# Performance work log

Hardware: AMD Instinct MI355X
Metric: run time of the kernel (lower is better)

Reference implementation:

```python
import jax, jax.numpy as jnp
import numpy as np

N_NODES = 50000
N_EDGES = 800000
IN_CH = 128
OUT_CH = 32
HID = 2 * OUT_CH  # 64


def gcn_layer(x, W, b, src, dst, n):
    """PyG GCNConv: x' = D^-1/2 (A + I) D^-1/2 (x W) + b, flow source->target."""
    h = x @ W  # [n, out]
    # degree on target nodes, +1 for self loop
    deg = jax.ops.segment_sum(jnp.ones(dst.shape[0], h.dtype), dst, num_segments=n) + 1.0
    dis = jax.lax.rsqrt(deg)  # deg^-1/2
    norm = dis[src] * dis[dst]  # [E]
    msg = h[src] * norm[:, None]  # gather + scale, [E, out]
    agg = jax.ops.segment_sum(msg, dst, num_segments=n)  # scatter-add
    # self-loop contribution has norm dis[i]*dis[i] = 1/deg[i]
    return agg + h * (dis * dis)[:, None] + b


def setup_inputs() -> dict:
    key = jax.random.key(0)
    k1, k2, k3, k4, k5, k6 = jax.random.split(key, 6)
    x = jax.random.normal(k1, (N_NODES, IN_CH), dtype=jnp.float32)
    edge_index = jax.random.randint(k2, (2, N_EDGES), 0, N_NODES, dtype=jnp.int64)
    # Glorot-style init for GCN weights
    W1 = jax.random.normal(k3, (IN_CH, HID), dtype=jnp.float32) / np.sqrt(IN_CH)
    b1 = jnp.zeros((HID,), dtype=jnp.float32)
    W2 = jax.random.normal(k4, (HID, OUT_CH), dtype=jnp.float32) / np.sqrt(HID)
    b2 = jnp.zeros((OUT_CH,), dtype=jnp.float32)
    return {"x": x, "W1": W1, "b1": b1, "W2": W2, "b2": b2, "edge_index": edge_index}


def reference(x, W1, b1, W2, b2, edge_index):
    src, dst = edge_index[0], edge_index[1]
    h = jax.nn.relu(gcn_layer(x, W1, b1, src, dst, N_NODES))
    out = gcn_layer(h, W2, b2, src, dst, N_NODES)
    return out
```

## Files before the change

kernel.cpp:

```cpp
#include <hip/hip_runtime.h>
#include <hip/hip_bf16.h>
#include <cstddef>
#include <cstdint>

#define N_NODES 50000
#define N_EDGES 800000
#define IN_CH 128
#define HID 64
#define OUT_CH 32

#define NBUCK 196
#define BCAP2 5120
#define NBLK 256
#define EPB 3125
#define NT1 782

typedef __attribute__((ext_vector_type(8))) short bf16x8;
typedef __attribute__((ext_vector_type(8))) unsigned short u16x8;
typedef __attribute__((ext_vector_type(4))) float f32x4;

__device__ __forceinline__ unsigned short bf16rne(float f) {
    union { float f; unsigned u; } c; c.f = f;
    unsigned r = c.u + 0x7FFF + ((c.u >> 16) & 1);
    return (unsigned short)(r >> 16);
}
__device__ __forceinline__ float bf16f(unsigned short b) {
    union { unsigned u; float f; } c; c.u = ((unsigned)b) << 16;
    return c.f;
}

__device__ __forceinline__ void load_edge(const void* ei, int flag, int e, int& s, int& d) {
    if (flag) {
        const long long* p = (const long long*)ei;
        s = (int)p[e];
        d = (int)p[e + N_EDGES];
    } else {
        const int* p = (const int*)ei;
        s = p[e];
        d = p[e + N_EDGES];
    }
}

__global__ __launch_bounds__(256) void zerocur_kernel(int* __restrict__ cursor) {
    if (threadIdx.x < NBUCK) cursor[threadIdx.x] = 0;
}

__global__ __launch_bounds__(256) void scatter1_kernel(const void* ei,
                                                       int* __restrict__ cursor,
                                                       unsigned* __restrict__ packed) {
    __shared__ unsigned cbuf[EPB];
    __shared__ int h[NBUCK];
    __shared__ int lcur[NBUCK];
    __shared__ unsigned red[256];
    const int t = threadIdx.x;
    const int base = blockIdx.x * EPB;

    {
        unsigned acc = 0;
        const unsigned* w = (const unsigned*)ei;
        for (int i = t; i < 2048; i += 256) acc |= w[2 * i + 1];
        red[t] = acc;
    }
    if (t < NBUCK) h[t] = 0;
    __syncthreads();
    if (t < 128) red[t] |= red[t + 128];
    __syncthreads();
    if (t < 64) red[t] |= red[t + 64];
    __syncthreads();
    if (t == 0) {
        unsigned q = 0;
        for (int i = 0; i < 64; ++i) q |= red[i];
        red[0] = q;
    }
    __syncthreads();
    const int flag = (red[0] == 0) ? 1 : 0;

    for (int i = t; i < EPB; i += 256) {
        int s, d;
        load_edge(ei, flag, base + i, s, d);
        cbuf[i] = (unsigned)s | ((unsigned)d << 16);
        atomicAdd(&h[d >> 8], 1);
    }
    __syncthreads();
    if (t < NBUCK) lcur[t] = h[t] ? (t * BCAP2 + atomicAdd(&cursor[t], h[t])) : 0;
    __syncthreads();
    for (int i = t; i < EPB; i += 256) {
        unsigned p = cbuf[i];
        int b = p >> 24;
        int pos = atomicAdd(&lcur[b], 1);
        packed[pos] = p;
    }
}

__global__ __launch_bounds__(256) void buckgemm1_kernel(
        const int* __restrict__ cursor, unsigned* __restrict__ packed,
        unsigned* __restrict__ rowinfo, float* __restrict__ dis,
        const float* __restrict__ x, const float* __restrict__ W1,
        unsigned short* __restrict__ h1b) {
    __shared__ union {
        struct { int cnt[256]; int pref[256]; int lbuf[BCAP2]; } bk;
        struct { unsigned short xa[64][136]; unsigned short wb[64][136]; } g1;
    } u;
    const int t = threadIdx.x;

    if (blockIdx.x < NBUCK) {
        const int b = blockIdx.x;
        const int nodebase = b << 8;
        const int rbase = b * BCAP2;
        const int bsize = cursor[b];
        const int nb = min(256, N_NODES - nodebase);

        u.bk.cnt[t] = 0;
        __syncthreads();
        for (int i = t; i < bsize; i += 256)
            atomicAdd(&u.bk.cnt[(packed[rbase + i] >> 16) & 255], 1);
        __syncthreads();
        const int deg = u.bk.cnt[t];
        u.bk.pref[t] = deg;
        __syncthreads();
        for (int off = 1; off < 256; off <<= 1) {
            int q = (t >= off) ? u.bk.pref[t - off] : 0;
            __syncthreads();
            u.bk.pref[t] += q;
            __syncthreads();
        }
        const int excl = u.bk.pref[t] - deg;
        if (t < nb) {
            rowinfo[nodebase + t] = (unsigned)(rbase + excl) | ((unsigned)deg << 20);
            dis[nodebase + t] = rsqrtf((float)deg + 1.0f);
        }
        __syncthreads();
        u.bk.cnt[t] = excl;
        __syncthreads();
        for (int i = t; i < bsize; i += 256) {
            unsigned p = packed[rbase + i];
            int pos = atomicAdd(&u.bk.cnt[(p >> 16) & 255], 1);
            u.bk.lbuf[pos] = (int)(p & 0xFFFFu);
        }
        __syncthreads();
        for (int i = t; i < bsize; i += 256)
            packed[rbase + i] = (unsigned)u.bk.lbuf[i];
    } else {
        const int w = t >> 6;
        const int l = t & 63;
        const int brow = (blockIdx.x - NBUCK) * 64;

        for (int f = t; f < 64 * 32; f += 256) {
            int r = f >> 5, c = (f & 31) << 2;
            int gr = brow + r;
            float4 v = (gr < N_NODES) ? *(const float4*)(x + gr * IN_CH + c)
                                      : make_float4(0.f, 0.f, 0.f, 0.f);
            u.g1.xa[r][c + 0] = bf16rne(v.x); u.g1.xa[r][c + 1] = bf16rne(v.y);
            u.g1.xa[r][c + 2] = bf16rne(v.z); u.g1.xa[r][c + 3] = bf16rne(v.w);
        }
        for (int f = t; f < 128 * 16; f += 256) {
            int k = f >> 4, n = (f & 15) << 2;
            float4 v = *(const float4*)(W1 + k * HID + n);
            u.g1.wb[n + 0][k] = bf16rne(v.x); u.g1.wb[n + 1][k] = bf16rne(v.y);
            u.g1.wb[n + 2][k] = bf16rne(v.z); u.g1.wb[n + 3][k] = bf16rne(v.w);
        }
        __syncthreads();

        const int fr = l & 15;
        const int fk = (l >> 4) << 3;
        f32x4 acc[4] = {{0.f,0.f,0.f,0.f},{0.f,0.f,0.f,0.f},
                        {0.f,0.f,0.f,0.f},{0.f,0.f,0.f,0.f}};
#pragma unroll
        for (int kb = 0; kb < 4; ++kb) {
            const int k = kb * 32 + fk;
            bf16x8 a = *(const bf16x8*)&u.g1.xa[w * 16 + fr][k];
#pragma unroll
            for (int n = 0; n < 4; ++n) {
                bf16x8 bfr = *(const bf16x8*)&u.g1.wb[n * 16 + fr][k];
                acc[n] = __builtin_amdgcn_mfma_f32_16x16x32_bf16(a, bfr, acc[n], 0, 0, 0);
            }
        }
        const int rb = brow + w * 16 + ((l >> 4) << 2);
#pragma unroll
        for (int n = 0; n < 4; ++n) {
#pragma unroll
            for (int i = 0; i < 4; ++i) {
                int r = rb + i;
                if (r < N_NODES) h1b[r * HID + n * 16 + fr] = bf16rne(acc[n][i]);
            }
        }
    }
}

__global__ __launch_bounds__(1024) void agg1gemm2_kernel(
        const unsigned* __restrict__ rowinfo, const unsigned* __restrict__ sorted,
        const float* __restrict__ dis, const unsigned short* __restrict__ h1b,
        const float* __restrict__ b1, const float* __restrict__ W2,
        unsigned short* __restrict__ h2b) {
    __shared__ unsigned short xa[64][72];
    __shared__ unsigned short wb[32][72];
    const int t = threadIdx.x;
    const int w = t >> 6;
    const int l = t & 63;
    const int g = l >> 3;
    const int cl = l & 7;
    const int base = blockIdx.x * 64;

    if (t < 512) {
        int k = t >> 3, n = (t & 7) << 2;
        float4 v = *(const float4*)(W2 + k * OUT_CH + n);
        wb[n + 0][k] = bf16rne(v.x); wb[n + 1][k] = bf16rne(v.y);
        wb[n + 2][k] = bf16rne(v.z); wb[n + 3][k] = bf16rne(v.w);
    }

#pragma unroll
    for (int q = 0; q < 4; ++q) {
        const int row = w * 4 + q;
        const int d = base + row;
        float a0 = 0.f, a1 = 0.f, a2 = 0.f, a3 = 0.f;
        float a4 = 0.f, a5 = 0.f, a6 = 0.f, a7 = 0.f;
        if (d < N_NODES) {
            const unsigned ri = rowinfo[d];
            const int beg = (int)(ri & 0xFFFFFu);
            const int end = beg + (int)(ri >> 20);
            const float dd = dis[d];
            for (int j = beg + g; j < end; j += 8) {
                int s = (int)sorted[j];
                float n = dis[s] * dd;
                bf16x8 h = *(const bf16x8*)(h1b + s * HID + 8 * cl);
                a0 += bf16f((unsigned short)h[0]) * n; a1 += bf16f((unsigned short)h[1]) * n;
                a2 += bf16f((unsigned short)h[2]) * n; a3 += bf16f((unsigned short)h[3]) * n;
                a4 += bf16f((unsigned short)h[4]) * n; a5 += bf16f((unsigned short)h[5]) * n;
                a6 += bf16f((unsigned short)h[6]) * n; a7 += bf16f((unsigned short)h[7]) * n;
            }
#pragma unroll
            for (int st = 8; st <= 32; st <<= 1) {
                a0 += __shfl_xor(a0, st, 64); a1 += __shfl_xor(a1, st, 64);
                a2 += __shfl_xor(a2, st, 64); a3 += __shfl_xor(a3, st, 64);
                a4 += __shfl_xor(a4, st, 64); a5 += __shfl_xor(a5, st, 64);
                a6 += __shfl_xor(a6, st, 64); a7 += __shfl_xor(a7, st, 64);
            }
            if (g == 0) {
                bf16x8 hs = *(const bf16x8*)(h1b + d * HID + 8 * cl);
                float4 bv0 = *(const float4*)(b1 + 8 * cl);
                float4 bv1 = *(const float4*)(b1 + 8 * cl + 4);
                const float dd2 = dd * dd;
                u16x8 o;
                o[0] = bf16rne(fmaxf(a0 + bf16f((unsigned short)hs[0]) * dd2 + bv0.x, 0.f));
                o[1] = bf16rne(fmaxf(a1 + bf16f((unsigned short)hs[1]) * dd2 + bv0.y, 0.f));
                o[2] = bf16rne(fmaxf(a2 + bf16f((unsigned short)hs[2]) * dd2 + bv0.z, 0.f));
                o[3] = bf16rne(fmaxf(a3 + bf16f((unsigned short)hs[3]) * dd2 + bv0.w, 0.f));
                o[4] = bf16rne(fmaxf(a4 + bf16f((unsigned short)hs[4]) * dd2 + bv1.x, 0.f));
                o[5] = bf16rne(fmaxf(a5 + bf16f((unsigned short)hs[5]) * dd2 + bv1.y, 0.f));
                o[6] = bf16rne(fmaxf(a6 + bf16f((unsigned short)hs[6]) * dd2 + bv1.z, 0.f));
                o[7] = bf16rne(fmaxf(a7 + bf16f((unsigned short)hs[7]) * dd2 + bv1.w, 0.f));
                *(u16x8*)&xa[row][8 * cl] = o;
            }
        } else if (g == 0) {
            u16x8 z = {0, 0, 0, 0, 0, 0, 0, 0};
            *(u16x8*)&xa[row][8 * cl] = z;
        }
    }
    __syncthreads();

    if (w < 8) {
        const int rt = (w >> 1) << 4;
        const int ct = (w & 1) << 4;
        const int fr = l & 15;
        const int fk = (l >> 4) << 3;
        f32x4 acc = {0.f, 0.f, 0.f, 0.f};
#pragma unroll
        for (int kb = 0; kb < 2; ++kb) {
            const int k = kb * 32 + fk;
            bf16x8 a = *(const bf16x8*)&xa[rt + fr][k];
            bf16x8 bfr = *(const bf16x8*)&wb[ct + fr][k];
            acc = __builtin_amdgcn_mfma_f32_16x16x32_bf16(a, bfr, acc, 0, 0, 0);
        }
        const int rb = base + rt + ((l >> 4) << 2);
#pragma unroll
        for (int i = 0; i < 4; ++i) {
            int r = rb + i;
            if (r < N_NODES) h2b[r * OUT_CH + ct + fr] = bf16rne(acc[i]);
        }
    }
}

__global__ __launch_bounds__(256) void agg2_kernel(
        const unsigned* __restrict__ rowinfo, const unsigned* __restrict__ sorted,
        const float* __restrict__ dis, const unsigned short* __restrict__ h2b,
        const float* __restrict__ b2, float* __restrict__ out) {
    const int l = threadIdx.x & 63;
    const int g = l >> 2;
    const int cl = l & 3;
    const int d = blockIdx.x * 4 + (threadIdx.x >> 6);
    if (d >= N_NODES) return;
    const unsigned ri = rowinfo[d];
    const int beg = (int)(ri & 0xFFFFFu);
    const int end = beg + (int)(ri >> 20);
    const float dd = dis[d];
    float a0 = 0.f, a1 = 0.f, a2 = 0.f, a3 = 0.f;
    float a4 = 0.f, a5 = 0.f, a6 = 0.f, a7 = 0.f;
    for (int j = beg + g; j < end; j += 16) {
        int s = (int)sorted[j];
        float n = dis[s] * dd;
        bf16x8 h = *(const bf16x8*)(h2b + s * OUT_CH + 8 * cl);
        a0 += bf16f((unsigned short)h[0]) * n; a1 += bf16f((unsigned short)h[1]) * n;
        a2 += bf16f((unsigned short)h[2]) * n; a3 += bf16f((unsigned short)h[3]) * n;
        a4 += bf16f((unsigned short)h[4]) * n; a5 += bf16f((unsigned short)h[5]) * n;
        a6 += bf16f((unsigned short)h[6]) * n; a7 += bf16f((unsigned short)h[7]) * n;
    }
#pragma unroll
    for (int st = 4; st <= 32; st <<= 1) {
        a0 += __shfl_xor(a0, st, 64); a1 += __shfl_xor(a1, st, 64);
        a2 += __shfl_xor(a2, st, 64); a3 += __shfl_xor(a3, st, 64);
        a4 += __shfl_xor(a4, st, 64); a5 += __shfl_xor(a5, st, 64);
        a6 += __shfl_xor(a6, st, 64); a7 += __shfl_xor(a7, st, 64);
    }
    if (g == 0) {
        bf16x8 hs = *(const bf16x8*)(h2b + d * OUT_CH + 8 * cl);
        float4 bv0 = *(const float4*)(b2 + 8 * cl);
        float4 bv1 = *(const float4*)(b2 + 8 * cl + 4);
        float d2 = dd * dd;
        float4 o0, o1;
        o0.x = a0 + bf16f((unsigned short)hs[0]) * d2 + bv0.x;
        o0.y = a1 + bf16f((unsigned short)hs[1]) * d2 + bv0.y;
        o0.z = a2 + bf16f((unsigned short)hs[2]) * d2 + bv0.z;
        o0.w = a3 + bf16f((unsigned short)hs[3]) * d2 + bv0.w;
        o1.x = a4 + bf16f((unsigned short)hs[4]) * d2 + bv1.x;
        o1.y = a5 + bf16f((unsigned short)hs[5]) * d2 + bv1.y;
        o1.z = a6 + bf16f((unsigned short)hs[6]) * d2 + bv1.z;
        o1.w = a7 + bf16f((unsigned short)hs[7]) * d2 + bv1.w;
        *(float4*)(out + d * OUT_CH + 8 * cl) = o0;
        *(float4*)(out + d * OUT_CH + 8 * cl + 4) = o1;
    }
}

extern "C" void kernel_launch(void* const* d_in, const int* in_sizes, int n_in,
                              void* d_out, int out_size, void* d_ws, size_t ws_size,
                              hipStream_t stream) {
    const float* x  = (const float*)d_in[0];
    const float* W1 = (const float*)d_in[1];
    const float* b1 = (const float*)d_in[2];
    const float* W2 = (const float*)d_in[3];
    const float* b2 = (const float*)d_in[4];
    const void*  ei = d_in[5];
    float* out = (float*)d_out;

    char* wp = (char*)d_ws;
    auto alloc = [&](size_t n) { char* p = wp; wp += (n + 511) & ~(size_t)511; return p; };
    int*   cursor  = (int*)alloc(NBUCK * 4);
    unsigned* rowinfo = (unsigned*)alloc((size_t)N_NODES * 4);
    float* dis     = (float*)alloc((size_t)N_NODES * 4);
    unsigned* packed = (unsigned*)alloc((size_t)NBUCK * BCAP2 * 4);
    unsigned short* h1b = (unsigned short*)alloc((size_t)N_NODES * HID * 2);
    unsigned short* h2b = (unsigned short*)alloc((size_t)N_NODES * OUT_CH * 2);

    zerocur_kernel<<<1, 256, 0, stream>>>(cursor);
    scatter1_kernel<<<NBLK, 256, 0, stream>>>(ei, cursor, packed);
    buckgemm1_kernel<<<NBUCK + NT1, 256, 0, stream>>>(cursor, packed, rowinfo, dis,
                                                      x, W1, h1b);
    agg1gemm2_kernel<<<NT1, 1024, 0, stream>>>(rowinfo, packed, dis, h1b, b1, W2, h2b);
    agg2_kernel<<<(N_NODES + 3) / 4, 256, 0, stream>>>(rowinfo, packed, dis, h2b, b2, out);
}
```

Measured before the change: 91.51 us.

## Prescale features by source deg^-1/2 to drop per-edge dis gathers

Factors the symmetric normalization so each feature row is pre-multiplied by its source node's dis: h1 is scaled by a new elementwise kernel, and h2 is scaled in the gemm2 epilogue. The aggregation loops then sum raw rows without gathering dis[s] per edge, and multiply by dis[d] once at the end. The layer-1 gather loop is also unrolled by two to keep more loads in flight. This costs an extra kernel launch plus a read and write of h1, and adds one more bf16 rounding of the scaled values.

Result: slower. 94.39 us (+3.1%).

```diff
diff --git a/kernel.cpp b/kernel.cpp
--- a/kernel.cpp
+++ b/kernel.cpp
@@ -185,6 +185,20 @@
             }
         }
     }
+}
+
+__global__ __launch_bounds__(256) void scaleh1_kernel(const float* __restrict__ dis,
+                                                      unsigned short* __restrict__ h1b) {
+    const int i = blockIdx.x * 256 + threadIdx.x;
+    if (i >= N_NODES * 8) return;
+    const int node = i >> 3;
+    const int part = (i & 7) << 3;
+    const float dd = dis[node];
+    u16x8 v = *(const u16x8*)(h1b + node * HID + part);
+    u16x8 o;
+#pragma unroll
+    for (int c = 0; c < 8; ++c) o[c] = bf16rne(bf16f(v[c]) * dd);
+    *(u16x8*)(h1b + node * HID + part) = o;
 }
 
 __global__ __launch_bounds__(1024) void agg1gemm2_kernel(
@@ -219,14 +233,28 @@
             const int beg = (int)(ri & 0xFFFFFu);
             const int end = beg + (int)(ri >> 20);
             const float dd = dis[d];
-            for (int j = beg + g; j < end; j += 8) {
-                int s = (int)sorted[j];
-                float n = dis[s] * dd;
-                bf16x8 h = *(const bf16x8*)(h1b + s * HID + 8 * cl);
-                a0 += bf16f((unsigned short)h[0]) * n; a1 += bf16f((unsigned short)h[1]) * n;
-                a2 += bf16f((unsigned short)h[2]) * n; a3 += bf16f((unsigned short)h[3]) * n;
-                a4 += bf16f((unsigned short)h[4]) * n; a5 += bf16f((unsigned short)h[5]) * n;
-                a6 += bf16f((unsigned short)h[6]) * n; a7 += bf16f((unsigned short)h[7]) * n;
+            int j = beg + g;
+            for (; j + 8 < end; j += 16) {
+                int s0 = (int)sorted[j];
+                int s1 = (int)sorted[j + 8];
+                bf16x8 h0 = *(const bf16x8*)(h1b + s0 * HID + 8 * cl);
+                bf16x8 h1v = *(const bf16x8*)(h1b + s1 * HID + 8 * cl);
+                a0 += bf16f((unsigned short)h0[0]); a1 += bf16f((unsigned short)h0[1]);
+                a2 += bf16f((unsigned short)h0[2]); a3 += bf16f((unsigned short)h0[3]);
+                a4 += bf16f((unsigned short)h0[4]); a5 += bf16f((unsigned short)h0[5]);
+                a6 += bf16f((unsigned short)h0[6]); a7 += bf16f((unsigned short)h0[7]);
+                a0 += bf16f((unsigned short)h1v[0]); a1 += bf16f((unsigned short)h1v[1]);
+                a2 += bf16f((unsigned short)h1v[2]); a3 += bf16f((unsigned short)h1v[3]);
+                a4 += bf16f((unsigned short)h1v[4]); a5 += bf16f((unsigned short)h1v[5]);
+                a6 += bf16f((unsigned short)h1v[6]); a7 += bf16f((unsigned short)h1v[7]);
+            }
+            if (j < end) {
+                int s0 = (int)sorted[j];
+                bf16x8 h0 = *(const bf16x8*)(h1b + s0 * HID + 8 * cl);
+                a0 += bf16f((unsigned short)h0[0]); a1 += bf16f((unsigned short)h0[1]);
+                a2 += bf16f((unsigned short)h0[2]); a3 += bf16f((unsigned short)h0[3]);
+                a4 += bf16f((unsigned short)h0[4]); a5 += bf16f((unsigned short)h0[5]);
+                a6 += bf16f((unsigned short)h0[6]); a7 += bf16f((unsigned short)h0[7]);
             }
 #pragma unroll
             for (int st = 8; st <= 32; st <<= 1) {
@@ -239,16 +267,15 @@
                 bf16x8 hs = *(const bf16x8*)(h1b + d * HID + 8 * cl);
                 float4 bv0 = *(const float4*)(b1 + 8 * cl);
                 float4 bv1 = *(const float4*)(b1 + 8 * cl + 4);
-                const float dd2 = dd * dd;
                 u16x8 o;
-                o[0] = bf16rne(fmaxf(a0 + bf16f((unsigned short)hs[0]) * dd2 + bv0.x, 0.f));
-                o[1] = bf16rne(fmaxf(a1 + bf16f((unsigned short)hs[1]) * dd2 + bv0.y, 0.f));
-                o[2] = bf16rne(fmaxf(a2 + bf16f((unsigned short)hs[2]) * dd2 + bv0.z, 0.f));
-                o[3] = bf16rne(fmaxf(a3 + bf16f((unsigned short)hs[3]) * dd2 + bv0.w, 0.f));
-                o[4] = bf16rne(fmaxf(a4 + bf16f((unsigned short)hs[4]) * dd2 + bv1.x, 0.f));
-                o[5] = bf16rne(fmaxf(a5 + bf16f((unsigned short)hs[5]) * dd2 + bv1.y, 0.f));
-                o[6] = bf16rne(fmaxf(a6 + bf16f((unsigned short)hs[6]) * dd2 + bv1.z, 0.f));
-                o[7] = bf16rne(fmaxf(a7 + bf16f((unsigned short)hs[7]) * dd2 + bv1.w, 0.f));
+                o[0] = bf16rne(fmaxf(dd * (a0 + bf16f((unsigned short)hs[0])) + bv0.x, 0.f));
+                o[1] = bf16rne(fmaxf(dd * (a1 + bf16f((unsigned short)hs[1])) + bv0.y, 0.f));
+                o[2] = bf16rne(fmaxf(dd * (a2 + bf16f((unsigned short)hs[2])) + bv0.z, 0.f));
+                o[3] = bf16rne(fmaxf(dd * (a3 + bf16f((unsigned short)hs[3])) + bv0.w, 0.f));
+                o[4] = bf16rne(fmaxf(dd * (a4 + bf16f((unsigned short)hs[4])) + bv1.x, 0.f));
+                o[5] = bf16rne(fmaxf(dd * (a5 + bf16f((unsigned short)hs[5])) + bv1.y, 0.f));
+                o[6] = bf16rne(fmaxf(dd * (a6 + bf16f((unsigned short)hs[6])) + bv1.z, 0.f));
+                o[7] = bf16rne(fmaxf(dd * (a7 + bf16f((unsigned short)hs[7])) + bv1.w, 0.f));
                 *(u16x8*)&xa[row][8 * cl] = o;
             }
         } else if (g == 0) {
@@ -275,7 +302,7 @@
 #pragma unroll
         for (int i = 0; i < 4; ++i) {
             int r = rb + i;
-            if (r < N_NODES) h2b[r * OUT_CH + ct + fr] = bf16rne(acc[i]);
+            if (r < N_NODES) h2b[r * OUT_CH + ct + fr] = bf16rne(acc[i] * dis[r]);
         }
     }
 }
@@ -297,12 +324,11 @@
     float a4 = 0.f, a5 = 0.f, a6 = 0.f, a7 = 0.f;
     for (int j = beg + g; j < end; j += 16) {
         int s = (int)sorted[j];
-        float n = dis[s] * dd;
         bf16x8 h = *(const bf16x8*)(h2b + s * OUT_CH + 8 * cl);
-        a0 += bf16f((unsigned short)h[0]) * n; a1 += bf16f((unsigned short)h[1]) * n;
-        a2 += bf16f((unsigned short)h[2]) * n; a3 += bf16f((unsigned short)h[3]) * n;
-        a4 += bf16f((unsigned short)h[4]) * n; a5 += bf16f((unsigned short)h[5]) * n;
-        a6 += bf16f((unsigned short)h[6]) * n; a7 += bf16f((unsigned short)h[7]) * n;
+        a0 += bf16f((unsigned short)h[0]); a1 += bf16f((unsigned short)h[1]);
+        a2 += bf16f((unsigned short)h[2]); a3 += bf16f((unsigned short)h[3]);
+        a4 += bf16f((unsigned short)h[4]); a5 += bf16f((unsigned short)h[5]);
+        a6 += bf16f((unsigned short)h[6]); a7 += bf16f((unsigned short)h[7]);
     }
 #pragma unroll
     for (int st = 4; st <= 32; st <<= 1) {
@@ -315,16 +341,15 @@
         bf16x8 hs = *(const bf16x8*)(h2b + d * OUT_CH + 8 * cl);
         float4 bv0 = *(const float4*)(b2 + 8 * cl);
         float4 bv1 = *(const float4*)(b2 + 8 * cl + 4);
-        float d2 = dd * dd;
         float4 o0, o1;
-        o0.x = a0 + bf16f((unsigned short)hs[0]) * d2 + bv0.x;
-        o0.y = a1 + bf16f((unsigned short)hs[1]) * d2 + bv0.y;
-        o0.z = a2 + bf16f((unsigned short)hs[2]) * d2 + bv0.z;
-        o0.w = a3 + bf16f((unsigned short)hs[3]) * d2 + bv0.w;
-        o1.x = a4 + bf16f((unsigned short)hs[4]) * d2 + bv1.x;
-        o1.y = a5 + bf16f((unsigned short)hs[5]) * d2 + bv1.y;
-        o1.z = a6 + bf16f((unsigned short)hs[6]) * d2 + bv1.z;
-        o1.w = a7 + bf16f((unsigned short)hs[7]) * d2 + bv1.w;
+        o0.x = dd * (a0 + bf16f((unsigned short)hs[0])) + bv0.x;
+        o0.y = dd * (a1 + bf16f((unsigned short)hs[1])) + bv0.y;
+        o0.z = dd * (a2 + bf16f((unsigned short)hs[2])) + bv0.z;
+        o0.w = dd * (a3 + bf16f((unsigned short)hs[3])) + bv0.w;
+        o1.x = dd * (a4 + bf16f((unsigned short)hs[4])) + bv1.x;
+        o1.y = dd * (a5 + bf16f((unsigned short)hs[5])) + bv1.y;
+        o1.z = dd * (a6 + bf16f((unsigned short)hs[6])) + bv1.z;
+        o1.w = dd * (a7 + bf16f((unsigned short)hs[7])) + bv1.w;
         *(float4*)(out + d * OUT_CH + 8 * cl) = o0;
         *(float4*)(out + d * OUT_CH + 8 * cl + 4) = o1;
     }
@@ -354,6 +379,7 @@
     scatter1_kernel<<<NBLK, 256, 0, stream>>>(ei, cursor, packed);
     buckgemm1_kernel<<<NBUCK + NT1, 256, 0, stream>>>(cursor, packed, rowinfo, dis,
                                                       x, W1, h1b);
+    scaleh1_kernel<<<(N_NODES * 8 + 255) / 256, 256, 0, stream>>>(dis, h1b);
     agg1gemm2_kernel<<<NT1, 1024, 0, stream>>>(rowinfo, packed, dis, h1b, b1, W2, h2b);
     agg2_kernel<<<(N_NODES + 3) / 4, 256, 0, stream>>>(rowinfo, packed, dis, h2b, b2, out);
 }
```
